# Performance work log

Hardware: AMD Instinct MI355X
Metric: run time of the kernel (lower is better)

The kernel has to match this reference:

```python
import jax, jax.numpy as jnp
import numpy as np

TEMPERATURE = 0.07


def setup_inputs() -> dict:
    key = jax.random.key(0)
    k1, k2 = jax.random.split(key)
    features = jax.random.normal(k1, (8192, 512), dtype=jnp.float32)
    targets = jax.random.randint(k2, (8192,), 0, 100, dtype=jnp.int64)
    return {"features": features, "targets": targets}


def reference(features, targets):
    n = features.shape[0]
    # L2 normalize along feature dim (F.normalize, dim=1)
    feats = features / jnp.linalg.norm(features, axis=1, keepdims=True)
    # [N, N] similarity matrix
    sim = jnp.matmul(feats, feats.T) / TEMPERATURE
    # positive-pair mask (same label, excluding self)
    mask = (targets[:, None] == targets[None, :]).astype(sim.dtype)
    mask = mask - jnp.eye(n, dtype=sim.dtype)
    # log_prob = sim - log(sum_j exp(sim_ij)) ; denominator includes the diagonal,
    # exactly as in the torch code. logsumexp is the stable single-pass form.
    log_prob = sim - jax.nn.logsumexp(sim, axis=1, keepdims=True)
    mean_log_prob_pos = jnp.sum(mask * log_prob, axis=1) / jnp.sum(mask, axis=1)
    loss = -jnp.mean(mean_log_prob_pos)
    return loss
```

## Files before the change

kernel.cpp:

```cpp
#include <hip/hip_runtime.h>

#define BM 128
#define BN 128
#define NSPLIT 8
#define TEMP 0.07f

typedef __attribute__((ext_vector_type(4))) float f32x4;

__global__ __launch_bounds__(256) void knorm(const float* __restrict__ X,
                                             unsigned char* __restrict__ Fq, int D) {
  int row = blockIdx.x * 4 + (threadIdx.x >> 6);
  int lane = threadIdx.x & 63;
  const float4* xr = (const float4*)(X + (size_t)row * D);
  float4 a = xr[lane * 2];
  float4 b = xr[lane * 2 + 1];
  float ss = a.x*a.x + a.y*a.y + a.z*a.z + a.w*a.w
           + b.x*b.x + b.y*b.y + b.z*b.z + b.w*b.w;
  #pragma unroll
  for (int off = 1; off < 64; off <<= 1) ss += __shfl_xor(ss, off, 64);
  float r = rsqrtf(ss);
  int lo = 0, hi = 0;
  lo = __builtin_amdgcn_cvt_pk_fp8_f32(a.x*r, a.y*r, lo, false);
  lo = __builtin_amdgcn_cvt_pk_fp8_f32(a.z*r, a.w*r, lo, true);
  hi = __builtin_amdgcn_cvt_pk_fp8_f32(b.x*r, b.y*r, hi, false);
  hi = __builtin_amdgcn_cvt_pk_fp8_f32(b.z*r, b.w*r, hi, true);
  int2 o = make_int2(lo, hi);
  *(int2*)(Fq + (size_t)row * D + lane * 8) = o;
}

__global__ __launch_bounds__(256, 1)
void kmain(const unsigned char* __restrict__ F, const int* __restrict__ tgt,
           float* __restrict__ psum, float* __restrict__ pmask, int N, int D) {
  __shared__ __align__(16) unsigned char Bs[BN * 512];

  const int tid  = threadIdx.x;
  const int lane = tid & 63;
  const int wave = tid >> 6;
  const int quad = lane >> 4;
  const int l15  = lane & 15;

  const int rowblk   = blockIdx.x / NSPLIT;
  const int split    = blockIdx.x % NSPLIT;
  const int rowbase  = rowblk * BM;
  const int colbase0 = split * (N / NSPLIT);

  long af[2][16];
  #pragma unroll
  for (int mi = 0; mi < 2; ++mi) {
    const unsigned char* rp = F + (size_t)(rowbase + wave*32 + mi*16 + l15) * 512 + quad*8;
    #pragma unroll
    for (int k = 0; k < 16; ++k)
      af[mi][k] = *(const long*)(rp + k * 32);
  }

  int trow[2][4];
  #pragma unroll
  for (int mi = 0; mi < 2; ++mi)
    #pragma unroll
    for (int r = 0; r < 4; ++r)
      trow[mi][r] = tgt[rowbase + wave*32 + mi*16 + quad*4 + r];

  float se[2][4], ms[2][4];
  #pragma unroll
  for (int mi = 0; mi < 2; ++mi)
    #pragma unroll
    for (int r = 0; r < 4; ++r) { se[mi][r] = 0.f; ms[mi][r] = 0.f; }

  const float C1 = (1.0f / TEMP) * 1.4426950408889634f;
  const float C0 = -C1;

  const int CT = (N / NSPLIT) / BN;
  for (int ct = 0; ct < CT; ++ct) {
    const int colbase = colbase0 + ct * BN;

    f32x4 acc[2][8];
    #pragma unroll
    for (int mi = 0; mi < 2; ++mi)
      #pragma unroll
      for (int ni = 0; ni < 8; ++ni)
        acc[mi][ni] = (f32x4){0.f, 0.f, 0.f, 0.f};

    __syncthreads();
    #pragma unroll
    for (int it = 0; it < 16; ++it) {
      const int L   = it * 256 + tid;
      const int row = L >> 5;
      const int ks  = (L & 31) ^ (row & 31);
      const unsigned char* g = F + (size_t)(colbase + row) * 512 + ks * 16;
      __builtin_amdgcn_global_load_lds(
          (const __attribute__((address_space(1))) void*)g,
          (__attribute__((address_space(3))) void*)(Bs + L * 16), 16, 0, 0);
    }
    __syncthreads();

    #pragma unroll
    for (int k = 0; k < 16; ++k) {
      #pragma unroll
      for (int ni = 0; ni < 8; ++ni) {
        const int row = ni*16 + l15;
        const int g8  = k*4 + quad;
        const int a   = row*512 + (((g8 >> 1) ^ (row & 31)) << 4) + (g8 & 1)*8;
        long b = *(const long*)(Bs + a);
        acc[0][ni] = __builtin_amdgcn_mfma_f32_16x16x32_fp8_fp8(af[0][k], b, acc[0][ni], 0, 0, 0);
        acc[1][ni] = __builtin_amdgcn_mfma_f32_16x16x32_fp8_fp8(af[1][k], b, acc[1][ni], 0, 0, 0);
      }
    }

    int tc[8];
    #pragma unroll
    for (int ni = 0; ni < 8; ++ni) tc[ni] = tgt[colbase + ni*16 + l15];
    #pragma unroll
    for (int mi = 0; mi < 2; ++mi)
      #pragma unroll
      for (int ni = 0; ni < 8; ++ni)
        #pragma unroll
        for (int r = 0; r < 4; ++r) {
          float v = acc[mi][ni][r];
          se[mi][r] += __builtin_amdgcn_exp2f(fmaf(v, C1, C0));
          if (tc[ni] == trow[mi][r]) ms[mi][r] += v;
        }
  }

  #pragma unroll
  for (int mi = 0; mi < 2; ++mi)
    #pragma unroll
    for (int r = 0; r < 4; ++r) {
      float s = se[mi][r], m = ms[mi][r];
      #pragma unroll
      for (int off = 1; off < 16; off <<= 1) {
        s += __shfl_xor(s, off, 64);
        m += __shfl_xor(m, off, 64);
      }
      if (l15 == 0) {
        int row = rowbase + wave*32 + mi*16 + quad*4 + r;
        psum[(size_t)split * N + row]  = s;
        pmask[(size_t)split * N + row] = m;
      }
    }
}

__global__ __launch_bounds__(256) void kfinal(
    const float* __restrict__ psum, const float* __restrict__ pmask,
    const int* __restrict__ tgt, float* __restrict__ out, int N) {
  __shared__ int h[128];
  __shared__ float wsum[4];
  const int tid = threadIdx.x;
  if (tid < 128) h[tid] = 0;
  __syncthreads();
  for (int i = tid; i < N; i += 256) atomicAdd(&h[tgt[i] & 127], 1);
  __syncthreads();

  const int i = blockIdx.x * 256 + tid;
  float s = 0.f, m = 0.f;
  #pragma unroll
  for (int sp = 0; sp < NSPLIT; ++sp) {
    s += psum[(size_t)sp * N + i];
    m += pmask[(size_t)sp * N + i];
  }
  const float invT = 1.0f / TEMP;
  float cnt = (float)(h[tgt[i] & 127] - 1);
  float term = (m - 1.0f) * invT / cnt - (logf(s) + invT);
  #pragma unroll
  for (int off = 1; off < 64; off <<= 1) term += __shfl_xor(term, off, 64);
  if ((tid & 63) == 0) wsum[tid >> 6] = term;
  __syncthreads();
  if (tid == 0)
    atomicAdd(out, -(wsum[0] + wsum[1] + wsum[2] + wsum[3]) / (float)N);
}

extern "C" void kernel_launch(void* const* d_in, const int* in_sizes, int n_in,
                              void* d_out, int out_size, void* d_ws, size_t ws_size,
                              hipStream_t stream) {
  const float* X  = (const float*)d_in[0];
  const int* tgt  = (const int*)d_in[1];
  float* out      = (float*)d_out;
  const int N = in_sizes[1];
  const int D = in_sizes[0] / N;

  char* w = (char*)d_ws;
  unsigned char* Fq = (unsigned char*)w;
  size_t off = (size_t)N * D;
  float* psum  = (float*)(w + off); off += (size_t)NSPLIT * N * sizeof(float);
  float* pmask = (float*)(w + off);

  hipMemsetAsync(d_out, 0, sizeof(float), stream);
  knorm<<<N / 4, 256, 0, stream>>>(X, Fq, D);
  kmain<<<(N / BM) * NSPLIT, 256, 0, stream>>>(Fq, tgt, psum, pmask, N, D);
  kfinal<<<N / 256, 256, 0, stream>>>(psum, pmask, tgt, out, N);
}
```

Measured before the change: 143.3 us.

## Fuse final reduction into main kernel via last-block counter, stagger column tiles

Removes the memset and the separate final kernel: each main-kernel block increments a global counter, and the last block to finish performs the histogram, per-row combination and final mean, writing the output directly. The counter is reset inside the normalization kernel. Column-tile iteration order is rotated per group of row blocks to spread concurrent reads across different column tiles, and the k loop unroll is reduced to 2. The single last block does the whole final reduction serially over all rows, which adds tail latency.

```diff
diff --git a/kernel.cpp b/kernel.cpp
--- a/kernel.cpp
+++ b/kernel.cpp
@@ -8,7 +8,9 @@
 typedef __attribute__((ext_vector_type(4))) float f32x4;
 
 __global__ __launch_bounds__(256) void knorm(const float* __restrict__ X,
-                                             unsigned char* __restrict__ Fq, int D) {
+                                             unsigned char* __restrict__ Fq,
+                                             int* __restrict__ done, int D) {
+  if (blockIdx.x == 0 && threadIdx.x == 0) *done = 0;
   int row = blockIdx.x * 4 + (threadIdx.x >> 6);
   int lane = threadIdx.x & 63;
   const float4* xr = (const float4*)(X + (size_t)row * D);
@@ -30,8 +32,12 @@
 
 __global__ __launch_bounds__(256, 1)
 void kmain(const unsigned char* __restrict__ F, const int* __restrict__ tgt,
-           float* __restrict__ psum, float* __restrict__ pmask, int N, int D) {
+           float* __restrict__ psum, float* __restrict__ pmask,
+           int* __restrict__ done, float* __restrict__ out, int N) {
   __shared__ __align__(16) unsigned char Bs[BN * 512];
+  __shared__ int h[128];
+  __shared__ float wsum[4];
+  __shared__ int lastFlag;
 
   const int tid  = threadIdx.x;
   const int lane = tid & 63;
@@ -43,6 +49,7 @@
   const int split    = blockIdx.x % NSPLIT;
   const int rowbase  = rowblk * BM;
   const int colbase0 = split * (N / NSPLIT);
+  const int phase    = ((rowblk >> 5) & 1) * 4;
 
   long af[2][16];
   #pragma unroll
@@ -60,17 +67,15 @@
     for (int r = 0; r < 4; ++r)
       trow[mi][r] = tgt[rowbase + wave*32 + mi*16 + quad*4 + r];
 
-  float se[2][4], ms[2][4];
-  #pragma unroll
-  for (int mi = 0; mi < 2; ++mi)
-    #pragma unroll
-    for (int r = 0; r < 4; ++r) { se[mi][r] = 0.f; ms[mi][r] = 0.f; }
+  float se[2][4] = {{0.f,0.f,0.f,0.f},{0.f,0.f,0.f,0.f}};
+  float ms[2][4] = {{0.f,0.f,0.f,0.f},{0.f,0.f,0.f,0.f}};
 
   const float C1 = (1.0f / TEMP) * 1.4426950408889634f;
   const float C0 = -C1;
 
   const int CT = (N / NSPLIT) / BN;
-  for (int ct = 0; ct < CT; ++ct) {
+  for (int t = 0; t < CT; ++t) {
+    const int ct = (t + phase) & 7;
     const int colbase = colbase0 + ct * BN;
 
     f32x4 acc[2][8];
@@ -93,7 +98,7 @@
     }
     __syncthreads();
 
-    #pragma unroll
+    #pragma unroll 2
     for (int k = 0; k < 16; ++k) {
       #pragma unroll
       for (int ni = 0; ni < 8; ++ni) {
@@ -137,35 +142,37 @@
         pmask[(size_t)split * N + row] = m;
       }
     }
-}
 
-__global__ __launch_bounds__(256) void kfinal(
-    const float* __restrict__ psum, const float* __restrict__ pmask,
-    const int* __restrict__ tgt, float* __restrict__ out, int N) {
-  __shared__ int h[128];
-  __shared__ float wsum[4];
-  const int tid = threadIdx.x;
+  __threadfence();
+  __syncthreads();
+  if (tid == 0) lastFlag = (atomicAdd(done, 1) == (N / BM) * NSPLIT - 1);
+  __syncthreads();
+  if (!lastFlag) return;
+  __threadfence();
+
   if (tid < 128) h[tid] = 0;
   __syncthreads();
   for (int i = tid; i < N; i += 256) atomicAdd(&h[tgt[i] & 127], 1);
   __syncthreads();
 
-  const int i = blockIdx.x * 256 + tid;
-  float s = 0.f, m = 0.f;
+  const float invT = 1.0f / TEMP;
+  float local = 0.f;
+  for (int i = tid; i < N; i += 256) {
+    float s = 0.f, m = 0.f;
+    #pragma unroll
+    for (int sp = 0; sp < NSPLIT; ++sp) {
+      s += psum[(size_t)sp * N + i];
+      m += pmask[(size_t)sp * N + i];
+    }
+    float cnt = (float)(h[tgt[i] & 127] - 1);
+    local += (m - 1.0f) * invT / cnt - (logf(s) + invT);
+  }
   #pragma unroll
-  for (int sp = 0; sp < NSPLIT; ++sp) {
-    s += psum[(size_t)sp * N + i];
-    m += pmask[(size_t)sp * N + i];
-  }
-  const float invT = 1.0f / TEMP;
-  float cnt = (float)(h[tgt[i] & 127] - 1);
-  float term = (m - 1.0f) * invT / cnt - (logf(s) + invT);
-  #pragma unroll
-  for (int off = 1; off < 64; off <<= 1) term += __shfl_xor(term, off, 64);
-  if ((tid & 63) == 0) wsum[tid >> 6] = term;
+  for (int off = 1; off < 64; off <<= 1) local += __shfl_xor(local, off, 64);
+  if (lane == 0) wsum[wave] = local;
   __syncthreads();
   if (tid == 0)
-    atomicAdd(out, -(wsum[0] + wsum[1] + wsum[2] + wsum[3]) / (float)N);
+    out[0] = -(wsum[0] + wsum[1] + wsum[2] + wsum[3]) / (float)N;
 }
 
 extern "C" void kernel_launch(void* const* d_in, const int* in_sizes, int n_in,
@@ -181,10 +188,9 @@
   unsigned char* Fq = (unsigned char*)w;
   size_t off = (size_t)N * D;
   float* psum  = (float*)(w + off); off += (size_t)NSPLIT * N * sizeof(float);
-  float* pmask = (float*)(w + off);
+  float* pmask = (float*)(w + off); off += (size_t)NSPLIT * N * sizeof(float);
+  int* done    = (int*)(w + off);
 
-  hipMemsetAsync(d_out, 0, sizeof(float), stream);
-  knorm<<<N / 4, 256, 0, stream>>>(X, Fq, D);
-  kmain<<<(N / BM) * NSPLIT, 256, 0, stream>>>(Fq, tgt, psum, pmask, N, D);
-  kfinal<<<N / 256, 256, 0, stream>>>(psum, pmask, tgt, out, N);
+  knorm<<<N / 4, 256, 0, stream>>>(X, Fq, done, D);
+  kmain<<<(N / BM) * NSPLIT, 256, 0, stream>>>(Fq, tgt, psum, pmask, done, out, N);
 }
```

After: 225.9 us. +57.7%, slower.
